# Kernel optimization log

Measured on AMD Instinct MI355X. Metric: run time of the kernel, lower is better.

The kernel has to match this reference:

```python
import jax, jax.numpy as jnp
import numpy as np

B, T, D, H = 2, 2048, 1024, 16
HD = D // H  # head_size = 64
EPS = 1e-5


def _layernorm(x, g, b):
    mu = jnp.mean(x, axis=-1, keepdims=True)
    var = jnp.mean(jnp.square(x - mu), axis=-1, keepdims=True)
    return (x - mu) * jax.lax.rsqrt(var + EPS) * g + b


def setup_inputs() -> dict:
    key = jax.random.key(0)
    ks = jax.random.split(key, 16)
    s = 0.02
    return {
        "x": jax.random.normal(ks[0], (B, T, D), jnp.float32),
        # per-head Q/K/V linears, stacked over heads: [H, D, HD] (in,out layout)
        "wq": jax.random.normal(ks[1], (H, D, HD), jnp.float32) * s,
        "bq": jnp.zeros((H, HD), jnp.float32),
        "wk": jax.random.normal(ks[2], (H, D, HD), jnp.float32) * s,
        "bk": jnp.zeros((H, HD), jnp.float32),
        "wv": jax.random.normal(ks[3], (H, D, HD), jnp.float32) * s,
        "bv": jnp.zeros((H, HD), jnp.float32),
        "wp": jax.random.normal(ks[4], (D, D), jnp.float32) * s,
        "bp": jnp.zeros((D,), jnp.float32),
        "w1": jax.random.normal(ks[5], (D, 4 * D), jnp.float32) * s,
        "b1": jnp.zeros((4 * D,), jnp.float32),
        "w2": jax.random.normal(ks[6], (4 * D, D), jnp.float32) * s,
        "b2": jnp.zeros((D,), jnp.float32),
        "ln1_g": jnp.ones((D,), jnp.float32),
        "ln1_b": jnp.zeros((D,), jnp.float32),
        "lnf_g": jnp.ones((D,), jnp.float32),
        "lnf_b": jnp.zeros((D,), jnp.float32),
        "ln2_g": jnp.ones((D,), jnp.float32),
        "ln2_b": jnp.zeros((D,), jnp.float32),
    }


def reference(x, wq, bq, wk, bk, wv, bv, wp, bp, w1, b1, w2, b2,
              ln1_g, ln1_b, lnf_g, lnf_b, ln2_g, ln2_b):
    b_, t_, d_ = x.shape
    # batched per-head projections: [B,H,T,HD]
    Q = jnp.einsum('btd,hde->bhte', x, wq) + bq[None, :, None, :]
    K = jnp.einsum('btd,hde->bhte', x, wk) + bk[None, :, None, :]
    V = jnp.einsum('btd,hde->bhte', x, wv) + bv[None, :, None, :]
    # raw attention scores, scaled -- NOTE: no softmax, no mask (matches source)
    wei = jnp.einsum('bhte,bhse->bhts', Q, K) * (HD ** -0.5)
    attn = jnp.einsum('bhts,bhse->bhte', wei, V)  # [B,H,T,HD]
    # concat heads along last dim == [B,T,H*HD]
    cat = attn.transpose(0, 2, 1, 3).reshape(b_, t_, d_)
    Kc = K.transpose(0, 2, 1, 3).reshape(b_, t_, d_)
    Vc = V.transpose(0, 2, 1, 3).reshape(b_, t_, d_)
    out = cat @ wp + bp
    out1 = _layernorm(x + out, ln1_g, ln1_b)
    # FeedForward: ln(idx + net(idx)) internally
    ff = jax.nn.relu(out1 @ w1 + b1) @ w2 + b2
    ffo = _layernorm(out1 + ff, lnf_g, lnf_b)
    out2 = _layernorm(out1 + ffo, ln2_g, ln2_b)
    return (out2, Kc, Vc)
```

## Files before the change

kernel.cpp:

```cpp
#include <hip/hip_runtime.h>

typedef unsigned short u16;
typedef __attribute__((ext_vector_type(4))) float f32x4;
typedef __attribute__((ext_vector_type(8))) __bf16 bf16x8;
typedef __attribute__((ext_vector_type(8))) unsigned short u16x8;
typedef __attribute__((ext_vector_type(4))) unsigned short u16x4;

__device__ __forceinline__ u16 f2b(float f) {
    unsigned int u = __builtin_bit_cast(unsigned int, f);
    u = (u + 0x7FFFu + ((u >> 16) & 1u)) >> 16;
    return (u16)u;
}
__device__ __forceinline__ float b2f(u16 h) {
    unsigned int u = ((unsigned int)h) << 16;
    return __builtin_bit_cast(float, u);
}

__device__ __forceinline__ void gload_lds16(const u16* g, u16* l) {
    __builtin_amdgcn_global_load_lds(
        (const __attribute__((address_space(1))) void*)g,
        (__attribute__((address_space(3))) void*)l,
        16, 0, 0);
}

__device__ __forceinline__ bf16x8 lds_frag(const u16* p) {
    u16x8 t = *(const u16x8*)p;
    return __builtin_bit_cast(bf16x8, t);
}

#define FENCE asm volatile("" ::: "memory")
#define BARRIER do { FENCE; __builtin_amdgcn_s_barrier(); FENCE; \
                     __builtin_amdgcn_sched_barrier(0); } while (0)
#define SCHED0 __builtin_amdgcn_sched_barrier(0)
#define LGKM0 do { asm volatile("s_waitcnt lgkmcnt(0)" ::: "memory"); \
                   __builtin_amdgcn_sched_barrier(0); } while (0)
#define WAIT_VM8 do { asm volatile("s_waitcnt vmcnt(8)" ::: "memory"); \
                      __builtin_amdgcn_sched_barrier(0); } while (0)
#define WAIT_VM0 do { asm volatile("s_waitcnt vmcnt(0)" ::: "memory"); \
                      __builtin_amdgcn_sched_barrier(0); } while (0)

__global__ __launch_bounds__(256) void cast_x_kernel(const float* __restrict__ in,
                                                     u16* __restrict__ out) {
    int i = (blockIdx.x * 256 + threadIdx.x) * 4;
    float4 v = *(const float4*)&in[i];
    u16x4 o = { f2b(v.x), f2b(v.y), f2b(v.z), f2b(v.w) };
    *(u16x4*)&out[i] = o;
}

__global__ __launch_bounds__(256) void tr_wqkv(const float* __restrict__ wq,
                                               const float* __restrict__ wk,
                                               const float* __restrict__ wv,
                                               u16* __restrict__ WT) {
    __shared__ float tile[32][33];
    int z = blockIdx.z;
    int sel = z >> 4, h = z & 15;
    const float* w = (sel == 0) ? wq : (sel == 1) ? wk : wv;
    w += (long)h * 65536;
    int tx = threadIdx.x & 31, ty = threadIdx.x >> 5;
    int d0 = blockIdx.x * 32, e0 = blockIdx.y * 32;
#pragma unroll
    for (int i = 0; i < 32; i += 8)
        tile[ty + i][tx] = w[(long)(d0 + ty + i) * 64 + e0 + tx];
    __syncthreads();
#pragma unroll
    for (int i = 0; i < 32; i += 8)
        WT[((long)(sel * 1024 + h * 64 + e0 + ty + i)) * 1024 + d0 + tx] = f2b(tile[tx][ty + i]);
}

__global__ __launch_bounds__(256) void transpose_cast3(
    const float* __restrict__ wp, const float* __restrict__ w1, const float* __restrict__ w2,
    const float* __restrict__ bq, const float* __restrict__ bk, const float* __restrict__ bv,
    u16* __restrict__ WPT, u16* __restrict__ W1T, u16* __restrict__ W2T,
    float* __restrict__ BI) {
    int bid = blockIdx.x;
    if (bid >= 9216) {
        int i = (bid - 9216) * 256 + threadIdx.x;
        const float* b = (i < 1024) ? bq : (i < 2048) ? bk : bv;
        BI[i] = b[((i & 1023) >> 6) * 64 + (i & 63)];
        return;
    }
    const float* in; u16* out; int C, R, bx, by;
    if (bid < 1024)      { in = wp; out = WPT; R = 1024; C = 1024; bx = bid & 31;  by = bid >> 5; }
    else if (bid < 5120) { int b = bid - 1024; in = w1; out = W1T; R = 1024; C = 4096; bx = b & 127; by = b >> 7; }
    else                 { int b = bid - 5120; in = w2; out = W2T; R = 4096; C = 1024; bx = b & 31;  by = b >> 5; }
    __shared__ float tile[32][33];
    int tx = threadIdx.x & 31, ty = threadIdx.x >> 5;
    int r0 = by * 32, c0 = bx * 32;
#pragma unroll
    for (int i = 0; i < 32; i += 8)
        tile[ty + i][tx] = in[(long)(r0 + ty + i) * C + c0 + tx];
    __syncthreads();
#pragma unroll
    for (int i = 0; i < 32; i += 8)
        out[(long)(c0 + ty + i) * R + r0 + tx] = f2b(tile[tx][ty + i]);
}

template <int MODE, int WM, int WN, int MF, int NF, bool COLOUT>
__global__ __launch_bounds__(WM * WN * 64, 2) void gemmT(
    const u16* __restrict__ A, const u16* __restrict__ BT, const float* __restrict__ bias,
    u16* __restrict__ Cb, float* __restrict__ KV,
    u16* __restrict__ Q0, u16* __restrict__ Q1,
    int M, int N, int K, int lda, int ldb, int ldc, int kchunk) {
    constexpr int T   = WM * WN * 64;
    constexpr int BM  = WM * MF * 16;
    constexpr int BN  = WN * NF * 16;
    constexpr int RPI = T / 8;
    constexpr int LA  = BM / RPI;
    constexpr int LB  = BN / RPI;
    constexpr int EPI = T * 8;
    constexpr int MFH = MF / 2;
    constexpr int ASZ = BM * 64, BSZ = BN * 64;
    __shared__ __align__(16) u16 SMEM[2 * ASZ + 2 * BSZ];
    u16* As0 = SMEM;
    u16* As1 = SMEM + ASZ;
    u16* Bs0 = SMEM + 2 * ASZ;
    u16* Bs1 = SMEM + 2 * ASZ + BSZ;
    const int tid = threadIdx.x;
    const int lane = tid & 63;
    const int wid = tid >> 6;
    const int wr = wid / WN, wc = wid % WN;
    const int ntile = N / BN;
    const int mtile = M / BM;
    int bid = blockIdx.x;
    int kb = 0, ksz = K;
    u16* Pout = Q0;
    if (MODE == 4) {
        int tiles = mtile * ntile;
        int sk = bid / tiles; bid -= sk * tiles;
        kb = sk * kchunk;
        int rem = K - kb; ksz = rem < kchunk ? rem : kchunk;
        Pout = sk ? Q1 : Q0;
    }
    {
        int q = (mtile * ntile) >> 3;
        bid = (bid & 7) * q + (bid >> 3);
    }
    int bi, bj;
    if (COLOUT) { bj = bid / mtile; bi = bid % mtile; }
    else        { bi = bid / ntile; bj = bid % ntile; }
    const int brow = bi * BM, bcol = bj * BN;
    const int nt = ksz >> 6;

    const int srow = tid >> 3;
    const int scol = ((tid & 7) ^ (srow & 7)) << 3;
    const u16* ag = A + (long)(brow + srow) * lda + kb + scol;
    const u16* bg = BT + (long)(bcol + srow) * ldb + kb + scol;
    const long aI = (long)RPI * lda, bI = (long)RPI * ldb;
    const int sdst = tid << 3;

    auto STAGE = [&](u16* lA, u16* lB, int t) {
#pragma unroll
        for (int j = 0; j < LA; ++j)
            gload_lds16(ag + ((long)t << 6) + j * aI, &lA[j * EPI + sdst]);
#pragma unroll
        for (int j = 0; j < LB; ++j)
            gload_lds16(bg + ((long)t << 6) + j * bI, &lB[j * EPI + sdst]);
    };

    f32x4 acc[MF][NF] = {};
    bf16x8 af0[MFH], af1[MFH], bf0[NF], bf1[NF];

    const int ln15 = lane & 15;
    const int eoff = (((lane >> 4) << 3) ^ ((lane & 7) << 3));
    const int arow0 = wr * (MF * 16) + ln15;
    const int brow0 = wc * (NF * 16) + ln15;

#define RD_A(dst, S, kh, mh)                                                   \
    _Pragma("unroll") for (int m4 = 0; m4 < MFH; ++m4)                         \
        dst[m4] = lds_frag(&(S)[((arow0 + (((mh) * MFH + m4) << 4)) << 6) +    \
                                (eoff ^ ((kh) << 5))]);
#define RD_B(dst, S, kh)                                                       \
    _Pragma("unroll") for (int n = 0; n < NF; ++n)                             \
        dst[n] = lds_frag(&(S)[((brow0 + (n << 4)) << 6) + (eoff ^ ((kh) << 5))]);
#define MM(a, b, mh) do {                                                      \
    __builtin_amdgcn_s_setprio(1);                                             \
    _Pragma("unroll") for (int m4 = 0; m4 < MFH; ++m4)                         \
        _Pragma("unroll") for (int n = 0; n < NF; ++n)                         \
            acc[(mh) * MFH + m4][n] = __builtin_amdgcn_mfma_f32_16x16x32_bf16( \
                a[m4], b[n], acc[(mh) * MFH + m4][n], 0, 0, 0);                \
    __builtin_amdgcn_s_setprio(0);                                             \
} while (0)

    STAGE(As0, Bs0, 0);
    if (nt > 1) { STAGE(As1, Bs1, 1); WAIT_VM8; } else { WAIT_VM0; }
    BARRIER;
    RD_B(bf0, Bs0, 0);
    RD_A(af0, As0, 0, 0);

    u16 *Ac = As0, *Bc = Bs0, *Ao = As1, *Bo = Bs1;
    for (int t = 0; t < nt; ++t) {
        const bool hasN = (t + 1 < nt);
        const bool hasNN = (t + 2 < nt);
        RD_A(af1, Ac, 0, 1);
        MM(af0, bf0, 0);
        SCHED0;
        RD_B(bf1, Bc, 1);
        RD_A(af0, Ac, 1, 0);
        MM(af1, bf0, 1);
        SCHED0;
        RD_A(af1, Ac, 1, 1);
        MM(af0, bf1, 0);
        WAIT_VM0;
        BARRIER;
        if (hasN) { RD_B(bf0, Bo, 0); RD_A(af0, Ao, 0, 0); }
        MM(af1, bf1, 1);
        BARRIER;
        if (hasNN) STAGE(Ac, Bc, t + 2);
        SCHED0;
        u16* tp;
        tp = Ac; Ac = Ao; Ao = tp;
        tp = Bc; Bc = Bo; Bo = tp;
    }

    const int crow0 = wr * (MF * 16), ccol0 = wc * (NF * 16);
#pragma unroll
    for (int m = 0; m < MF; ++m) {
        int rbase = crow0 + (m << 4) + ((lane >> 4) << 2);
#pragma unroll
        for (int n = 0; n < NF; ++n) {
            int col = ccol0 + (n << 4) + ln15;
            float bv = (MODE == 4) ? 0.f : bias[bcol + col];
#pragma unroll
            for (int r = 0; r < 4; ++r) {
                float v = acc[m][n][r] + bv;
                if (MODE == 2) v = v > 0.f ? v : 0.f;
                int row = rbase + r;
                SMEM[row * BN + (col ^ ((row & 7) << 3))] = f2b(v);
            }
        }
    }
    LGKM0;
    BARRIER;
    u16* outp = (MODE == 4) ? Pout : Cb;
    constexpr int CHT = BM * BN / 8 / T;
#pragma unroll
    for (int k = 0; k < CHT; ++k) {
        int c = tid + k * T;
        int row = c / (BN / 8), co = (c % (BN / 8)) * 8;
        u16x8 vv = *(const u16x8*)&SMEM[row * BN + (co ^ ((row & 7) << 3))];
        *(u16x8*)&outp[(long)(brow + row) * ldc + bcol + co] = vv;
        if (MODE == 1) {
            int cg = bcol + co;
            if (cg >= 1024) {
                int cc = cg - 1024;
                long kbase = (long)(cc >> 10) * 4194304 + (long)(brow + row) * 1024 + (cc & 1023);
                float4 f0 = { b2f(vv[0]), b2f(vv[1]), b2f(vv[2]), b2f(vv[3]) };
                float4 f1 = { b2f(vv[4]), b2f(vv[5]), b2f(vv[6]), b2f(vv[7]) };
                *(float4*)&KV[kbase] = f0;
                *(float4*)&KV[kbase + 4] = f1;
            }
        }
    }
#undef RD_A
#undef RD_B
#undef MM
}

__global__ __launch_bounds__(256) void ktv_partial(const u16* __restrict__ QKVB,
                                                   float* __restrict__ KTVF) {
    __shared__ __align__(16) u16 Ks[64 * 64];
    __shared__ __align__(16) u16 Vs[64 * 64];
    int tid = threadIdx.x;
    int tc = blockIdx.x, bh = blockIdx.y;
    int b = bh >> 4, h = bh & 15;
    int j = tid & 63, i0 = (tid >> 6) * 16;
    float acc[16] = {};
    for (int st = 0; st < 4; ++st) {
        int t0 = tc * 256 + st * 64;
        __syncthreads();
#pragma unroll
        for (int i = 0; i < 2; ++i) {
            int c = i * 256 + tid;
            long base = (long)(b * 2048 + t0 + (c >> 3)) * 3072 + h * 64 + (c & 7) * 8;
            *(u16x8*)&Ks[c * 8] = *(const u16x8*)&QKVB[base + 1024];
            *(u16x8*)&Vs[c * 8] = *(const u16x8*)&QKVB[base + 2048];
        }
        __syncthreads();
        for (int tt = 0; tt < 64; ++tt) {
            float vj = b2f(Vs[tt * 64 + j]);
            u16x8 k0 = *(const u16x8*)&Ks[tt * 64 + i0];
            u16x8 k1 = *(const u16x8*)&Ks[tt * 64 + i0 + 8];
#pragma unroll
            for (int r = 0; r < 8; ++r) acc[r] += b2f(k0[r]) * vj;
#pragma unroll
            for (int r = 0; r < 8; ++r) acc[r + 8] += b2f(k1[r]) * vj;
        }
    }
#pragma unroll
    for (int r = 0; r < 16; ++r)
        atomicAdd(&KTVF[bh * 4096 + (i0 + r) * 64 + j], acc[r]);
}

__global__ __launch_bounds__(256) void cast_ktv(const float* __restrict__ KTVF,
                                                u16* __restrict__ KTVT) {
    int idx = blockIdx.x * 256 + threadIdx.x;
    int bh = idx >> 12, r = idx & 4095;
    int n = r >> 6, k = r & 63;
    KTVT[idx] = f2b(KTVF[bh * 4096 + k * 64 + n] * 0.125f);
}

__global__ __launch_bounds__(256) void attn_gemm(const u16* __restrict__ QKVB,
                                                 const u16* __restrict__ KTVT,
                                                 u16* __restrict__ cat) {
    __shared__ __align__(16) u16 Qs[64 * 64];
    __shared__ __align__(16) u16 Bs[64 * 64];
    int tid = threadIdx.x, wid = tid >> 6, lane = tid & 63;
    int rt = blockIdx.x, bh = blockIdx.y;
    int b = bh >> 4, h = bh & 15;
    long qbase = (long)(b * 2048 + rt * 64) * 3072 + h * 64;
#pragma unroll
    for (int i = 0; i < 2; ++i) {
        int c = i * 256 + tid;
        gload_lds16(QKVB + qbase + (c >> 3) * 3072 + (c & 7) * 8, &Qs[(i * 256 + wid * 64) * 8]);
        gload_lds16(KTVT + bh * 4096 + c * 8, &Bs[(i * 256 + wid * 64) * 8]);
    }
    __syncthreads();
    f32x4 acc[4] = {};
#pragma unroll
    for (int kk = 0; kk < 2; ++kk) {
        bf16x8 a = lds_frag(&Qs[(wid * 16 + (lane & 15)) * 64 + kk * 32 + (lane >> 4) * 8]);
#pragma unroll
        for (int n = 0; n < 4; ++n) {
            bf16x8 bb = lds_frag(&Bs[(n * 16 + (lane & 15)) * 64 + kk * 32 + (lane >> 4) * 8]);
            acc[n] = __builtin_amdgcn_mfma_f32_16x16x32_bf16(a, bb, acc[n], 0, 0, 0);
        }
    }
#pragma unroll
    for (int n = 0; n < 4; ++n)
#pragma unroll
        for (int r = 0; r < 4; ++r) {
            int row = rt * 64 + wid * 16 + (lane >> 4) * 4 + r;
            int col = h * 64 + n * 16 + (lane & 15);
            cat[(long)(b * 2048 + row) * 1024 + col] = f2b(acc[n][r]);
        }
}

__device__ __forceinline__ void block_reduce2(float& a, float& b) {
    __syncthreads();
#pragma unroll
    for (int off = 32; off; off >>= 1) {
        a += __shfl_down(a, off);
        b += __shfl_down(b, off);
    }
    __shared__ float sa[4], sb[4];
    int wid = threadIdx.x >> 6, lane = threadIdx.x & 63;
    if (lane == 0) { sa[wid] = a; sb[wid] = b; }
    __syncthreads();
    a = sa[0] + sa[1] + sa[2] + sa[3];
    b = sb[0] + sb[1] + sb[2] + sb[3];
}

__global__ __launch_bounds__(256) void ln1_kernel(
    const float* __restrict__ x,
    const u16* __restrict__ q0, const u16* __restrict__ q1,
    const float* __restrict__ bp,
    const float* __restrict__ g, const float* __restrict__ bt,
    float* __restrict__ out1f, u16* __restrict__ out1b) {
    int row = blockIdx.x, tid = threadIdx.x;
    long base = (long)row * 1024 + tid * 4;
    float4 xv = *(const float4*)&x[base];
    u16x4 a0 = *(const u16x4*)&q0[base];
    u16x4 a1 = *(const u16x4*)&q1[base];
    float4 bb = *(const float4*)&bp[tid * 4];
    float xa[4] = { xv.x, xv.y, xv.z, xv.w };
    float bba[4] = { bb.x, bb.y, bb.z, bb.w };
    float s[4];
#pragma unroll
    for (int r = 0; r < 4; ++r)
        s[r] = xa[r] + b2f(a0[r]) + b2f(a1[r]) + bba[r];
    float sum = s[0] + s[1] + s[2] + s[3];
    float sq = s[0] * s[0] + s[1] * s[1] + s[2] * s[2] + s[3] * s[3];
    block_reduce2(sum, sq);
    float mu = sum * (1.f / 1024.f);
    float var = sq * (1.f / 1024.f) - mu * mu;
    float rs = rsqrtf(var + 1e-5f);
    float o0 = (s[0] - mu) * rs * g[tid * 4 + 0] + bt[tid * 4 + 0];
    float o1 = (s[1] - mu) * rs * g[tid * 4 + 1] + bt[tid * 4 + 1];
    float o2 = (s[2] - mu) * rs * g[tid * 4 + 2] + bt[tid * 4 + 2];
    float o3 = (s[3] - mu) * rs * g[tid * 4 + 3] + bt[tid * 4 + 3];
    float4 of; of.x = o0; of.y = o1; of.z = o2; of.w = o3;
    u16x4 ob = (u16x4){ f2b(o0), f2b(o1), f2b(o2), f2b(o3) };
    *(float4*)&out1f[base] = of;
    *(u16x4*)&out1b[base] = ob;
}

__global__ __launch_bounds__(256) void lnf_kernel(
    const float* __restrict__ out1f,
    const u16* __restrict__ q0, const u16* __restrict__ q1,
    const float* __restrict__ b2,
    const float* __restrict__ lnfg, const float* __restrict__ lnfb,
    const float* __restrict__ ln2g, const float* __restrict__ ln2b,
    float* __restrict__ out2) {
    int row = blockIdx.x, tid = threadIdx.x;
    long base = (long)row * 1024 + tid * 4;
    float4 o1 = *(const float4*)&out1f[base];
    u16x4 a0 = *(const u16x4*)&q0[base];
    u16x4 a1 = *(const u16x4*)&q1[base];
    float4 bb = *(const float4*)&b2[tid * 4];
    float o1a[4] = { o1.x, o1.y, o1.z, o1.w };
    float bba[4] = { bb.x, bb.y, bb.z, bb.w };
    float s1[4];
#pragma unroll
    for (int r = 0; r < 4; ++r)
        s1[r] = o1a[r] + b2f(a0[r]) + b2f(a1[r]) + bba[r];
    float sum = s1[0] + s1[1] + s1[2] + s1[3];
    float sq = s1[0] * s1[0] + s1[1] * s1[1] + s1[2] * s1[2] + s1[3] * s1[3];
    block_reduce2(sum, sq);
    float mu = sum * (1.f / 1024.f);
    float rs = rsqrtf(sq * (1.f / 1024.f) - mu * mu + 1e-5f);
    float s2[4];
#pragma unroll
    for (int r = 0; r < 4; ++r) {
        float ffo = (s1[r] - mu) * rs * lnfg[tid * 4 + r] + lnfb[tid * 4 + r];
        s2[r] = o1a[r] + ffo;
    }
    float sum2 = s2[0] + s2[1] + s2[2] + s2[3];
    float sq2 = s2[0] * s2[0] + s2[1] * s2[1] + s2[2] * s2[2] + s2[3] * s2[3];
    block_reduce2(sum2, sq2);
    float mu2 = sum2 * (1.f / 1024.f);
    float rs2 = rsqrtf(sq2 * (1.f / 1024.f) - mu2 * mu2 + 1e-5f);
    float4 o;
    o.x = (s2[0] - mu2) * rs2 * ln2g[tid * 4 + 0] + ln2b[tid * 4 + 0];
    o.y = (s2[1] - mu2) * rs2 * ln2g[tid * 4 + 1] + ln2b[tid * 4 + 1];
    o.z = (s2[2] - mu2) * rs2 * ln2g[tid * 4 + 2] + ln2b[tid * 4 + 2];
    o.w = (s2[3] - mu2) * rs2 * ln2g[tid * 4 + 3] + ln2b[tid * 4 + 3];
    *(float4*)&out2[base] = o;
}

extern "C" void kernel_launch(void* const* d_in, const int* in_sizes, int n_in,
                              void* d_out, int out_size, void* d_ws, size_t ws_size,
                              hipStream_t stream) {
    const float* x    = (const float*)d_in[0];
    const float* wq   = (const float*)d_in[1];
    const float* bq   = (const float*)d_in[2];
    const float* wk   = (const float*)d_in[3];
    const float* bk   = (const float*)d_in[4];
    const float* wv   = (const float*)d_in[5];
    const float* bv   = (const float*)d_in[6];
    const float* wp   = (const float*)d_in[7];
    const float* bp   = (const float*)d_in[8];
    const float* w1   = (const float*)d_in[9];
    const float* b1   = (const float*)d_in[10];
    const float* w2   = (const float*)d_in[11];
    const float* b2   = (const float*)d_in[12];
    const float* ln1g = (const float*)d_in[13];
    const float* ln1b = (const float*)d_in[14];
    const float* lnfg = (const float*)d_in[15];
    const float* lnfb = (const float*)d_in[16];
    const float* ln2g = (const float*)d_in[17];
    const float* ln2b = (const float*)d_in[18];

    float* out2 = (float*)d_out;
    float* kv   = (float*)d_out + 4194304;

    char* ws = (char*)d_ws;
    u16*   XB     = (u16*)  (ws + 0);
    u16*   CAT    = XB;
    u16*   WQKVT  = (u16*)  (ws + 8388608);
    float* BQKV   = (float*)(ws + 14680064);
    u16*   WPT    = (u16*)  (ws + 14692352);
    u16*   W1T    = (u16*)  (ws + 16789504);
    u16*   W2T    = (u16*)  (ws + 25178112);
    float* KTVF   = (float*)(ws + 33566720);
    u16*   KTVT   = (u16*)  (ws + 34091008);
    u16*   QKVB   = (u16*)  (ws + 34353152);
    u16*   OUT1B  = QKVB;
    u16*   Q3_0   = (u16*)  (ws + 59518976);
    u16*   Q3_1   = (u16*)  (ws + 67907584);
    float* OUT1F  = (float*)(ws + 76296192);
    u16*   H1     = (u16*)  (ws + 93073408);
    u16*   Q5_0   = (u16*)  (ws + 0);
    u16*   Q5_1   = (u16*)  (ws + 34353152);
    (void)ws_size; (void)in_sizes; (void)n_in; (void)out_size;

    hipMemsetAsync(KTVF, 0, 32 * 4096 * 4, stream);
    cast_x_kernel<<<4096, 256, 0, stream>>>(x, XB);
    tr_wqkv<<<dim3(32, 2, 48), 256, 0, stream>>>(wq, wk, wv, WQKVT);
    transpose_cast3<<<9228, 256, 0, stream>>>(wp, w1, w2, bq, bk, bv,
                                              WPT, W1T, W2T, BQKV);

    gemmT<1, 2, 4, 4, 6, true><<<256, 512, 0, stream>>>(
        XB, WQKVT, BQKV, QKVB, kv, nullptr, nullptr,
        4096, 3072, 1024, 1024, 1024, 3072, 0);
    ktv_partial<<<dim3(8, 32), 256, 0, stream>>>(QKVB, KTVF);
    cast_ktv<<<512, 256, 0, stream>>>(KTVF, KTVT);
    attn_gemm<<<dim3(32, 32), 256, 0, stream>>>(QKVB, KTVT, CAT);

    gemmT<4, 2, 2, 4, 4, false><<<512, 256, 0, stream>>>(
        CAT, WPT, nullptr, nullptr, nullptr, Q3_0, Q3_1,
        4096, 1024, 1024, 1024, 1024, 1024, 512);
    ln1_kernel<<<4096, 256, 0, stream>>>(x, Q3_0, Q3_1, bp, ln1g, ln1b, OUT1F, OUT1B);

    gemmT<2, 2, 2, 4, 4, false><<<1024, 256, 0, stream>>>(
        OUT1B, W1T, b1, H1, nullptr, nullptr, nullptr,
        4096, 4096, 1024, 1024, 1024, 4096, 0);
    gemmT<4, 2, 2, 4, 4, false><<<512, 256, 0, stream>>>(
        H1, W2T, nullptr, nullptr, nullptr, Q5_0, Q5_1,
        4096, 1024, 4096, 4096, 4096, 1024, 2048);
    lnf_kernel<<<4096, 256, 0, stream>>>(OUT1F, Q5_0, Q5_1, b2,
                                         lnfg, lnfb, ln2g, ln2b, out2);
}
```

Baseline: 207.6 us.

## Fold per-head K^T V into the output projection weights, dropping attention GEMM

Result: no change. 205.0 us (-1.2%).

```diff
diff --git a/kernel.cpp b/kernel.cpp
--- a/kernel.cpp
+++ b/kernel.cpp
@@ -124,7 +124,7 @@
     int bid = blockIdx.x;
     int kb = 0, ksz = K;
     u16* Pout = Q0;
-    if (MODE == 4) {
+    if (MODE == 4 || MODE == 5) {
         int tiles = mtile * ntile;
         int sk = bid / tiles; bid -= sk * tiles;
         kb = sk * kchunk;
@@ -140,11 +140,13 @@
     else        { bi = bid / ntile; bj = bid % ntile; }
     const int brow = bi * BM, bcol = bj * BN;
     const int nt = ksz >> 6;
+    const u16* BTe = BT;
+    if (MODE == 5 && brow >= (M >> 1)) BTe = (const u16*)Cb;
 
     const int srow = tid >> 3;
     const int scol = ((tid & 7) ^ (srow & 7)) << 3;
     const u16* ag = A + (long)(brow + srow) * lda + kb + scol;
-    const u16* bg = BT + (long)(bcol + srow) * ldb + kb + scol;
+    const u16* bg = BTe + (long)(bcol + srow) * ldb + kb + scol;
     const long aI = (long)RPI * lda, bI = (long)RPI * ldb;
     const int sdst = tid << 3;
 
@@ -219,7 +221,7 @@
 #pragma unroll
         for (int n = 0; n < NF; ++n) {
             int col = ccol0 + (n << 4) + ln15;
-            float bv = (MODE == 4) ? 0.f : bias[bcol + col];
+            float bv = (MODE == 4 || MODE == 5) ? 0.f : bias[bcol + col];
 #pragma unroll
             for (int r = 0; r < 4; ++r) {
                 float v = acc[m][n][r] + bv;
@@ -231,7 +233,7 @@
     }
     LGKM0;
     BARRIER;
-    u16* outp = (MODE == 4) ? Pout : Cb;
+    u16* outp = (MODE == 4 || MODE == 5) ? Pout : Cb;
     constexpr int CHT = BM * BN / 8 / T;
 #pragma unroll
     for (int k = 0; k < CHT; ++k) {
@@ -291,48 +293,57 @@
         atomicAdd(&KTVF[bh * 4096 + (i0 + r) * 64 + j], acc[r]);
 }
 
-__global__ __launch_bounds__(256) void cast_ktv(const float* __restrict__ KTVF,
-                                                u16* __restrict__ KTVT) {
-    int idx = blockIdx.x * 256 + threadIdx.x;
-    int bh = idx >> 12, r = idx & 4095;
-    int n = r >> 6, k = r & 63;
-    KTVT[idx] = f2b(KTVF[bh * 4096 + k * 64 + n] * 0.125f);
-}
-
-__global__ __launch_bounds__(256) void attn_gemm(const u16* __restrict__ QKVB,
-                                                 const u16* __restrict__ KTVT,
-                                                 u16* __restrict__ cat) {
-    __shared__ __align__(16) u16 Qs[64 * 64];
-    __shared__ __align__(16) u16 Bs[64 * 64];
-    int tid = threadIdx.x, wid = tid >> 6, lane = tid & 63;
-    int rt = blockIdx.x, bh = blockIdx.y;
+__global__ __launch_bounds__(256) void wpb_kernel(const float* __restrict__ KTVF,
+                                                  const u16* __restrict__ WPT,
+                                                  u16* __restrict__ WPBT) {
+    __shared__ __align__(16) u16 Ks[64 * 72];
+    int tid = threadIdx.x, lane = tid & 63, w = tid >> 6;
+    int jt = blockIdx.x, bh = blockIdx.y;
     int b = bh >> 4, h = bh & 15;
-    long qbase = (long)(b * 2048 + rt * 64) * 3072 + h * 64;
-#pragma unroll
-    for (int i = 0; i < 2; ++i) {
-        int c = i * 256 + tid;
-        gload_lds16(QKVB + qbase + (c >> 3) * 3072 + (c & 7) * 8, &Qs[(i * 256 + wid * 64) * 8]);
-        gload_lds16(KTVT + bh * 4096 + c * 8, &Bs[(i * 256 + wid * 64) * 8]);
+    const float* kt = KTVF + bh * 4096;
+    {
+        int idx = tid * 16;
+        int e = idx >> 6, ep = idx & 63;
+        float4 v0 = *(const float4*)&kt[idx];
+        float4 v1 = *(const float4*)&kt[idx + 4];
+        float4 v2 = *(const float4*)&kt[idx + 8];
+        float4 v3 = *(const float4*)&kt[idx + 12];
+        u16x8 o0 = { f2b(v0.x * 0.125f), f2b(v0.y * 0.125f), f2b(v0.z * 0.125f), f2b(v0.w * 0.125f),
+                     f2b(v1.x * 0.125f), f2b(v1.y * 0.125f), f2b(v1.z * 0.125f), f2b(v1.w * 0.125f) };
+        u16x8 o1 = { f2b(v2.x * 0.125f), f2b(v2.y * 0.125f), f2b(v2.z * 0.125f), f2b(v2.w * 0.125f),
+                     f2b(v3.x * 0.125f), f2b(v3.y * 0.125f), f2b(v3.z * 0.125f), f2b(v3.w * 0.125f) };
+        *(u16x8*)&Ks[e * 72 + ep] = o0;
+        *(u16x8*)&Ks[e * 72 + ep + 8] = o1;
     }
     __syncthreads();
-    f32x4 acc[4] = {};
-#pragma unroll
-    for (int kk = 0; kk < 2; ++kk) {
-        bf16x8 a = lds_frag(&Qs[(wid * 16 + (lane & 15)) * 64 + kk * 32 + (lane >> 4) * 8]);
+    int ln15 = lane & 15, l4 = lane >> 4;
+    bf16x8 bf[4][2];
+#pragma unroll
+    for (int n = 0; n < 4; ++n)
+#pragma unroll
+        for (int kh = 0; kh < 2; ++kh)
+            bf[n][kh] = lds_frag(&Ks[(n * 16 + ln15) * 72 + kh * 32 + l4 * 8]);
+    int j0 = jt * 256 + w * 64;
+    f32x4 acc[4][4] = {};
+#pragma unroll
+    for (int m = 0; m < 4; ++m) {
+        const u16* ap = &WPT[(long)(j0 + m * 16 + ln15) * 1024 + h * 64 + l4 * 8];
+        bf16x8 a0 = __builtin_bit_cast(bf16x8, *(const u16x8*)ap);
+        bf16x8 a1 = __builtin_bit_cast(bf16x8, *(const u16x8*)(ap + 32));
 #pragma unroll
         for (int n = 0; n < 4; ++n) {
-            bf16x8 bb = lds_frag(&Bs[(n * 16 + (lane & 15)) * 64 + kk * 32 + (lane >> 4) * 8]);
-            acc[n] = __builtin_amdgcn_mfma_f32_16x16x32_bf16(a, bb, acc[n], 0, 0, 0);
+            acc[m][n] = __builtin_amdgcn_mfma_f32_16x16x32_bf16(a0, bf[n][0], acc[m][n], 0, 0, 0);
+            acc[m][n] = __builtin_amdgcn_mfma_f32_16x16x32_bf16(a1, bf[n][1], acc[m][n], 0, 0, 0);
         }
     }
 #pragma unroll
-    for (int n = 0; n < 4; ++n)
-#pragma unroll
-        for (int r = 0; r < 4; ++r) {
-            int row = rt * 64 + wid * 16 + (lane >> 4) * 4 + r;
-            int col = h * 64 + n * 16 + (lane & 15);
-            cat[(long)(b * 2048 + row) * 1024 + col] = f2b(acc[n][r]);
-        }
+    for (int m = 0; m < 4; ++m)
+#pragma unroll
+        for (int n = 0; n < 4; ++n)
+#pragma unroll
+            for (int r = 0; r < 4; ++r)
+                WPBT[(long)b * 1048576 + (long)(j0 + m * 16 + l4 * 4 + r) * 1024 +
+                     h * 64 + n * 16 + ln15] = f2b(acc[m][n][r]);
 }
 
 __device__ __forceinline__ void block_reduce2(float& a, float& b) {
@@ -455,14 +466,13 @@
 
     char* ws = (char*)d_ws;
     u16*   XB     = (u16*)  (ws + 0);
-    u16*   CAT    = XB;
+    u16*   WPBT   = XB;
     u16*   WQKVT  = (u16*)  (ws + 8388608);
     float* BQKV   = (float*)(ws + 14680064);
     u16*   WPT    = (u16*)  (ws + 14692352);
     u16*   W1T    = (u16*)  (ws + 16789504);
     u16*   W2T    = (u16*)  (ws + 25178112);
     float* KTVF   = (float*)(ws + 33566720);
-    u16*   KTVT   = (u16*)  (ws + 34091008);
     u16*   QKVB   = (u16*)  (ws + 34353152);
     u16*   OUT1B  = QKVB;
     u16*   Q3_0   = (u16*)  (ws + 59518976);
@@ -483,12 +493,11 @@
         XB, WQKVT, BQKV, QKVB, kv, nullptr, nullptr,
         4096, 3072, 1024, 1024, 1024, 3072, 0);
     ktv_partial<<<dim3(8, 32), 256, 0, stream>>>(QKVB, KTVF);
-    cast_ktv<<<512, 256, 0, stream>>>(KTVF, KTVT);
-    attn_gemm<<<dim3(32, 32), 256, 0, stream>>>(QKVB, KTVT, CAT);
-
-    gemmT<4, 2, 2, 4, 4, false><<<512, 256, 0, stream>>>(
-        CAT, WPT, nullptr, nullptr, nullptr, Q3_0, Q3_1,
-        4096, 1024, 1024, 1024, 1024, 1024, 512);
+    wpb_kernel<<<dim3(4, 32), 256, 0, stream>>>(KTVF, WPT, WPBT);
+
+    gemmT<5, 2, 2, 4, 4, false><<<512, 256, 0, stream>>>(
+        QKVB, WPBT, nullptr, (u16*)(WPBT + 1048576), nullptr, Q3_0, Q3_1,
+        4096, 1024, 1024, 3072, 1024, 1024, 512);
     ln1_kernel<<<4096, 256, 0, stream>>>(x, Q3_0, Q3_1, bp, ln1g, ln1b, OUT1F, OUT1B);
 
     gemmT<2, 2, 2, 4, 4, false><<<1024, 256, 0, stream>>>(
```
